# Optimization experiments

Hardware: AMD Instinct MI355X
Metric: run time of the kernel (lower is better)

Reference implementation:

```python
import jax, jax.numpy as jnp
import numpy as np

B, T, D = 8, 1024, 256
H, KD = 8, 256          # keras MHA built with key_dim=embed_dim -> per-head dim = D
FF = 1024
WIN = 64                # causal sliding window size
G = 2                   # num_global_tokens (last-k tokens of the sequence)
EPS = 1e-6
NEG = -1e9


def _mha(q_in, kv_in, Wq, bq, Wk, bk, Wv, bv, Wo, bo, mask=None):
    """Keras-style MultiHeadAttention. q_in:[B,Tq,D], kv_in:[B,Ts,D] -> [B,Tq,D]."""
    q = jnp.einsum('btd,dhk->bthk', q_in, Wq) + bq
    k = jnp.einsum('bsd,dhk->bshk', kv_in, Wk) + bk
    v = jnp.einsum('bsd,dhk->bshk', kv_in, Wv) + bv
    s = jnp.einsum('bthk,bshk->bhts', q, k) / jnp.sqrt(jnp.asarray(KD, q.dtype))
    if mask is not None:
        s = jnp.where(mask, s, jnp.asarray(NEG, s.dtype))
    a = jax.nn.softmax(s, axis=-1)
    o = jnp.einsum('bhts,bshk->bthk', a, v)
    return jnp.einsum('bthk,hkd->btd', o, Wo) + bo


def _ln(x, g, b):
    m = jnp.mean(x, axis=-1, keepdims=True)
    v = jnp.mean(jnp.square(x - m), axis=-1, keepdims=True)
    return (x - m) * jax.lax.rsqrt(v + EPS) * g + b


def setup_inputs() -> dict:
    key = jax.random.key(0)
    ks = jax.random.split(key, 32)
    sp = 1.0 / np.sqrt(D)   # proj fan-in D
    so = 1.0 / np.sqrt(H * KD)

    def mha_params(k0):
        k = jax.random.split(k0, 4)
        return dict(
            Wq=jax.random.normal(k[0], (D, H, KD), jnp.float32) * sp,
            Wk=jax.random.normal(k[1], (D, H, KD), jnp.float32) * sp,
            Wv=jax.random.normal(k[2], (D, H, KD), jnp.float32) * sp,
            Wo=jax.random.normal(k[3], (H, KD, D), jnp.float32) * so,
        )
    lp = mha_params(ks[1])
    gp = mha_params(ks[2])
    inp = {
        'x': jax.random.normal(ks[0], (B, T, D), jnp.float32),
        'lWq': lp['Wq'], 'lbq': jnp.zeros((H, KD), jnp.float32),
        'lWk': lp['Wk'], 'lbk': jnp.zeros((H, KD), jnp.float32),
        'lWv': lp['Wv'], 'lbv': jnp.zeros((H, KD), jnp.float32),
        'lWo': lp['Wo'], 'lbo': jnp.zeros((D,), jnp.float32),
        'gWq': gp['Wq'], 'gbq': jnp.zeros((H, KD), jnp.float32),
        'gWk': gp['Wk'], 'gbk': jnp.zeros((H, KD), jnp.float32),
        'gWv': gp['Wv'], 'gbv': jnp.zeros((H, KD), jnp.float32),
        'gWo': gp['Wo'], 'gbo': jnp.zeros((D,), jnp.float32),
        'fW1': jax.random.normal(ks[3], (D, FF), jnp.float32) * sp,
        'fb1': jnp.zeros((FF,), jnp.float32),
        'fW2': jax.random.normal(ks[4], (FF, D), jnp.float32) * (1.0 / np.sqrt(FF)),
        'fb2': jnp.zeros((D,), jnp.float32),
        'ln1_g': jnp.ones((D,), jnp.float32), 'ln1_b': jnp.zeros((D,), jnp.float32),
        'ln2_g': jnp.ones((D,), jnp.float32), 'ln2_b': jnp.zeros((D,), jnp.float32),
    }
    return inp


def reference(x, lWq, lbq, lWk, lbk, lWv, lbv, lWo, lbo,
              gWq, gbq, gWk, gbk, gWv, gbv, gWo, gbo,
              fW1, fb1, fW2, fb2, ln1_g, ln1_b, ln2_g, ln2_b):
    i = jnp.arange(T)[:, None]
    j = jnp.arange(T)[None, :]
    win_mask = (j <= i) & (j > i - WIN)            # [T,T]
    win_mask = win_mask[None, None]                # [1,1,T,T]

    # Local window attention (the original per-timestep loop, fused via mask).
    local = _mha(x, x, lWq, lbq, lWk, lbk, lWv, lbv, lWo, lbo, mask=win_mask)

    # Global tokens: last G tokens attend to full sequence, then tokens attend to them.
    g = x[:, T - G:, :]                            # [B,G,D]
    g2 = _mha(g, x, gWq, gbq, gWk, gbk, gWv, gbv, gWo, gbo)
    gx = _mha(x, g2, gWq, gbq, gWk, gbk, gWv, gbv, gWo, gbo)

    attn_out = local + gx
    out1 = _ln(x + attn_out, ln1_g, ln1_b)
    ffn = jnp.maximum(out1 @ fW1 + fb1, 0.0) @ fW2 + fb2
    return _ln(out1 + ffn, ln2_g, ln2_b)
```

## Files before the change

### kernel.cpp

```cpp
#include <hip/hip_runtime.h>
#include <hip/hip_bf16.h>

#define B_ 8
#define T_ 1024
#define D_ 256
#define H_ 8
#define KD_ 256
#define HK_ 2048
#define FF_ 1024
#define WIN_ 64
#define BT_ 8192
#define S6_ 6144

using bf16 = __hip_bfloat16;
typedef float f32x4 __attribute__((ext_vector_type(4)));
typedef short s16x8 __attribute__((ext_vector_type(8)));

__device__ inline float b2f(bf16 h) { return __bfloat162float(h); }
__device__ inline float bs2f(short s) {
    unsigned int u = ((unsigned int)(unsigned short)s) << 16;
    return __builtin_bit_cast(float, u);
}
__device__ inline float us2f(unsigned short s) {
    unsigned int u = ((unsigned int)s) << 16;
    return __builtin_bit_cast(float, u);
}
__device__ inline unsigned short fbits(float x) { bf16 h = __float2bfloat16(x); return __builtin_bit_cast(unsigned short, h); }

__device__ __forceinline__ void stage16(const void* g, void* l) {
    __builtin_amdgcn_global_load_lds((const __attribute__((address_space(1))) void*)g,
                                     (__attribute__((address_space(3))) void*)l, 16, 0, 0);
}

struct TJob { const float* in; bf16* out; int R; int C; int os; int tile_start; };
struct TJobs { TJob j[10]; int total; };

__global__ void transpose_all(TJobs js) {
    __shared__ float tile[32][33];
    int bid = blockIdx.x;
    int ji = 0;
    while (ji < 9 && bid >= js.j[ji + 1].tile_start) ji++;
    TJob jb = js.j[ji];
    int t = bid - jb.tile_start;
    int tiles_x = jb.C / 32;
    int cb = (t % tiles_x) * 32, rb = (t / tiles_x) * 32;
    for (int k = 0; k < 4; k++) {
        int r = threadIdx.y + k * 8;
        tile[r][threadIdx.x] = jb.in[(size_t)(rb + r) * jb.C + cb + threadIdx.x];
    }
    __syncthreads();
    for (int k = 0; k < 4; k++) {
        int r = threadIdx.y + k * 8;
        jb.out[(size_t)(cb + r) * jb.os + rb + threadIdx.x] = __float2bfloat16(tile[threadIdx.x][r]);
    }
}

__global__ __launch_bounds__(256) void concat_bias6(const float* a0, const float* a1, const float* a2,
                                                    float* out) {
    int i = blockIdx.x * 256 + threadIdx.x;
    int seg = i >> 11, off = i & 2047;
    out[i] = (seg == 0 ? a0 : seg == 1 ? a1 : a2)[off];
}

template <int MODE, int BN>
__global__ __launch_bounds__(256) void gemm128(const bf16* __restrict__ A, const bf16* __restrict__ Bt,
                                               const float* __restrict__ bias, bf16* __restrict__ C,
                                               int M, int N, int K) {
    constexpr int NF = BN / 32;
    constexpr int ABUF = 128 * 64;
    constexpr int BBUF = BN * 64;
    constexpr int BUFE = ABUF + BBUF;
    constexpr int EC = BN + 8;
    constexpr int ARENA_E = (2 * BUFE > 128 * EC) ? 2 * BUFE : 128 * EC;
    __shared__ __align__(16) bf16 arena[ARENA_E];
    const int tid = threadIdx.x;
    const int w = tid >> 6, l = tid & 63;
    const int m0 = blockIdx.y * 128, n0 = blockIdx.x * BN;
    const int wm = (w >> 1) * 64, wn = (w & 1) * (BN / 2);
    const int srow = w * 8 + (l >> 3);
    const int scol = ((l & 7) ^ (l >> 3)) * 8;
    const int ldsOff = w * 512;
    const int nt = K / 64;

    auto stageT = [&](int buf, int k0) {
        bf16* Ad = arena + buf * BUFE;
        bf16* Bd = Ad + ABUF;
#pragma unroll
        for (int j = 0; j < 4; j++)
            stage16(A + (size_t)(m0 + j * 32 + srow) * K + k0 + scol, &Ad[ldsOff + j * 2048]);
#pragma unroll
        for (int j = 0; j < NF; j++)
            stage16(Bt + (size_t)(n0 + j * 32 + srow) * K + k0 + scol, &Bd[ldsOff + j * 2048]);
    };

    f32x4 acc[4][NF] = {};
    stageT(0, 0);
    __syncthreads();
    int cur = 0;
    for (int t = 0; t < nt; t++) {
        if (t + 1 < nt) stageT(cur ^ 1, (t + 1) * 64);
        const bf16* As = arena + cur * BUFE;
        const bf16* Bs = As + ABUF;
#pragma unroll
        for (int ks = 0; ks < 2; ks++) {
            s16x8 a[4], b[NF];
#pragma unroll
            for (int mf = 0; mf < 4; mf++) {
                int ar = wm + mf * 16 + (l & 15);
                int ch = (ks * 4 + (l >> 4)) ^ (ar & 7);
                a[mf] = *(const s16x8*)&As[ar * 64 + ch * 8];
            }
#pragma unroll
            for (int nf = 0; nf < NF; nf++) {
                int br = wn + nf * 16 + (l & 15);
                int ch = (ks * 4 + (l >> 4)) ^ (br & 7);
                b[nf] = *(const s16x8*)&Bs[br * 64 + ch * 8];
            }
            __builtin_amdgcn_s_setprio(1);
#pragma unroll
            for (int mf = 0; mf < 4; mf++)
#pragma unroll
                for (int nf = 0; nf < NF; nf++)
                    acc[mf][nf] = __builtin_amdgcn_mfma_f32_16x16x32_bf16(a[mf], b[nf], acc[mf][nf], 0, 0, 0);
            __builtin_amdgcn_s_setprio(0);
        }
        __syncthreads();
        cur ^= 1;
    }
    bf16* Es = arena;
#pragma unroll
    for (int mf = 0; mf < 4; mf++)
#pragma unroll
        for (int nf = 0; nf < NF; nf++)
#pragma unroll
            for (int r = 0; r < 4; r++) {
                int row = wm + mf * 16 + (l >> 4) * 4 + r;
                int col = wn + nf * 16 + (l & 15);
                float v = acc[mf][nf][r] + bias[n0 + col];
                if (MODE == 2) v = fmaxf(v, 0.f);
                Es[row * EC + col] = __float2bfloat16(v);
            }
    __syncthreads();
    constexpr int RPC = BN / 8;
    constexpr int CPT = (128 * BN) / (256 * 8);
#pragma unroll
    for (int c = 0; c < CPT; c++) {
        int lin = c * 256 + tid;
        int row = lin / RPC, cc = lin - row * RPC;
        s16x8 v = *(const s16x8*)&Es[row * EC + cc * 8];
        *(s16x8*)(C + (size_t)(m0 + row) * N + n0 + cc * 8) = v;
    }
}

__global__ __launch_bounds__(256) void local_attn(const bf16* __restrict__ XW, bf16* __restrict__ O) {
    __shared__ bf16 U[256 * 72];
    __shared__ bf16 Ps[64][136];
    const int tid = threadIdx.x, l = tid & 63, w = tid >> 6;
    const int qt = blockIdx.x, bh = blockIdx.y;
    const int b = bh >> 3, h = bh & 7;
    const int qs = qt * 64;
    const int r0 = w * 16;
    const int lrow = tid >> 2, lc4 = (tid & 3) * 8;
    const size_t obase = (size_t)b * T_ * HK_ + h * KD_;

    s16x8 qa[8];
    {
        const bf16* qbase = XW + (size_t)(b * T_ + qs + r0 + (l & 15)) * S6_ + h * KD_ + (l >> 4) * 8;
#pragma unroll
        for (int ks = 0; ks < 8; ks++) qa[ks] = *(const s16x8*)(qbase + ks * 32);
    }

    bf16(*Ks)[264] = (bf16(*)[264])U;
    {
        int tk = qs - 64 + lrow;
        const bf16* krow = XW + (size_t)(b * T_ + tk) * S6_ + 2048 + h * KD_;
#pragma unroll
        for (int c = 0; c < 8; c++) {
            int col = lc4 + c * 32;
            uint4 val = {0, 0, 0, 0};
            if (tk >= 0) val = *(const uint4*)(krow + col);
            *(uint4*)&Ks[lrow][col] = val;
        }
    }
    __syncthreads();
    f32x4 sacc[8];
#pragma unroll
    for (int f = 0; f < 8; f++) sacc[f] = (f32x4){0.f, 0.f, 0.f, 0.f};
    __builtin_amdgcn_s_setprio(1);
#pragma unroll
    for (int nf = 0; nf < 4; nf++)
#pragma unroll
        for (int ks = 0; ks < 8; ks++) {
            s16x8 bb = *(const s16x8*)&Ks[nf * 16 + (l & 15)][ks * 32 + (l >> 4) * 8];
            sacc[nf] = __builtin_amdgcn_mfma_f32_16x16x32_bf16(qa[ks], bb, sacc[nf], 0, 0, 0);
        }
    __builtin_amdgcn_s_setprio(0);
    __syncthreads();
    {
        const bf16* krow = XW + (size_t)(b * T_ + qs + lrow) * S6_ + 2048 + h * KD_;
#pragma unroll
        for (int c = 0; c < 8; c++) {
            int col = lc4 + c * 32;
            *(uint4*)&Ks[lrow][col] = *(const uint4*)(krow + col);
        }
    }
    __syncthreads();
    __builtin_amdgcn_s_setprio(1);
#pragma unroll
    for (int nf = 0; nf < 4; nf++)
#pragma unroll
        for (int ks = 0; ks < 8; ks++) {
            s16x8 bb = *(const s16x8*)&Ks[nf * 16 + (l & 15)][ks * 32 + (l >> 4) * 8];
            sacc[4 + nf] = __builtin_amdgcn_mfma_f32_16x16x32_bf16(qa[ks], bb, sacc[4 + nf], 0, 0, 0);
        }
    __builtin_amdgcn_s_setprio(0);

    uint4 vreg[8];
    {
        int tk = qs - 64 + lrow;
        const bf16* vrow = XW + (size_t)(b * T_ + tk) * S6_ + 4096 + h * KD_;
#pragma unroll
        for (int c = 0; c < 8; c++) {
            uint4 v = {0, 0, 0, 0};
            if (tk >= 0) v = *(const uint4*)(vrow + lc4 + c * 32);
            vreg[c] = v;
        }
    }

#pragma unroll
    for (int r = 0; r < 4; r++) {
        int i = qs + r0 + (l >> 4) * 4 + r;
#pragma unroll
        for (int f = 0; f < 8; f++) {
            int j = qs - 64 + f * 16 + (l & 15);
            bool valid = (j >= 0) && (j <= i) && (j > i - WIN_);
            sacc[f][r] = valid ? sacc[f][r] * (1.f / 16.f) : -1e9f;
        }
        float mm = -1e30f;
#pragma unroll
        for (int f = 0; f < 8; f++) mm = fmaxf(mm, sacc[f][r]);
        mm = fmaxf(mm, __shfl_xor(mm, 1, 64));
        mm = fmaxf(mm, __shfl_xor(mm, 2, 64));
        mm = fmaxf(mm, __shfl_xor(mm, 4, 64));
        mm = fmaxf(mm, __shfl_xor(mm, 8, 64));
        float ss = 0.f;
#pragma unroll
        for (int f = 0; f < 8; f++) {
            float e = __expf(sacc[f][r] - mm);
            sacc[f][r] = e;
            ss += e;
        }
        ss += __shfl_xor(ss, 1, 64);
        ss += __shfl_xor(ss, 2, 64);
        ss += __shfl_xor(ss, 4, 64);
        ss += __shfl_xor(ss, 8, 64);
        float inv = 1.f / ss;
#pragma unroll
        for (int f = 0; f < 8; f++) sacc[f][r] *= inv;
    }
    __syncthreads();

    bf16(*VT)[72] = (bf16(*)[72])U;
#pragma unroll
    for (int f = 0; f < 8; f++)
#pragma unroll
        for (int r = 0; r < 4; r++)
            Ps[r0 + (l >> 4) * 4 + r][f * 16 + (l & 15)] = __float2bfloat16(sacc[f][r]);
#pragma unroll
    for (int c = 0; c < 8; c++) {
        int col = lc4 + c * 32;
        bf16 tmp[8];
        *(uint4*)tmp = vreg[c];
        for (int e = 0; e < 8; e++) VT[col + e][lrow] = tmp[e];
    }
    __syncthreads();
    {
        const bf16* vrow = XW + (size_t)(b * T_ + qs + lrow) * S6_ + 4096 + h * KD_;
#pragma unroll
        for (int c = 0; c < 8; c++) vreg[c] = *(const uint4*)(vrow + lc4 + c * 32);
    }

    f32x4 oacc[16];
#pragma unroll
    for (int nf = 0; nf < 16; nf++) oacc[nf] = (f32x4){0.f, 0.f, 0.f, 0.f};
    for (int kb = 0; kb < 2; kb++) {
#pragma unroll
        for (int ks = 0; ks < 2; ks++) {
            s16x8 a = *(const s16x8*)&Ps[r0 + (l & 15)][kb * 64 + ks * 32 + (l >> 4) * 8];
            __builtin_amdgcn_s_setprio(1);
#pragma unroll
            for (int nf = 0; nf < 16; nf++) {
                s16x8 bb = *(const s16x8*)&VT[nf * 16 + (l & 15)][ks * 32 + (l >> 4) * 8];
                oacc[nf] = __builtin_amdgcn_mfma_f32_16x16x32_bf16(a, bb, oacc[nf], 0, 0, 0);
            }
            __builtin_amdgcn_s_setprio(0);
        }
        if (kb == 0) {
            __syncthreads();
#pragma unroll
            for (int c = 0; c < 8; c++) {
                int col = lc4 + c * 32;
                bf16 tmp[8];
                *(uint4*)tmp = vreg[c];
                for (int e = 0; e < 8; e++) VT[col + e][lrow] = tmp[e];
            }
            __syncthreads();
        }
    }
#pragma unroll
    for (int nf = 0; nf < 16; nf++)
#pragma unroll
        for (int r = 0; r < 4; r++) {
            int row = r0 + (l >> 4) * 4 + r;
            int col = nf * 16 + (l & 15);
            O[obase + (size_t)(qs + row) * HK_ + col] = __float2bfloat16(oacc[nf][r]);
        }
}

__global__ __launch_bounds__(256) void qg_kernel(const float* __restrict__ x, const bf16* __restrict__ gwq_t,
                                                 const float* __restrict__ gbq, float* __restrict__ qg) {
    __shared__ float xs[256];
    int bi = blockIdx.x, ch = blockIdx.y, tid = threadIdx.x;
    int b = bi >> 1, i = bi & 1;
    xs[tid] = x[((size_t)b * T_ + (T_ - 2 + i)) * D_ + tid];
    __syncthreads();
    int hk = ch * 256 + tid;
    const bf16* wr = gwq_t + (size_t)hk * D_;
    float acc = gbq[hk];
    for (int c = 0; c < 32; c++) {
        s16x8 wv = *(const s16x8*)&wr[c * 8];
#pragma unroll
        for (int e = 0; e < 8; e++) acc += xs[c * 8 + e] * bs2f(wv[e]);
    }
    qg[(size_t)bi * HK_ + hk] = acc;
}

__global__ __launch_bounds__(256) void qk_kernel(const float* __restrict__ qg, const bf16* __restrict__ gwk_t,
                                                 const float* __restrict__ gbk, float* __restrict__ qk,
                                                 float* __restrict__ cb) {
    __shared__ float qgs[256];
    __shared__ float red[4];
    int bi = blockIdx.x, h = blockIdx.y, tid = threadIdx.x;
    qgs[tid] = qg[(size_t)bi * HK_ + h * 256 + tid];
    __syncthreads();
    float acc = 0.f;
    const bf16* wcol = gwk_t + (size_t)(h * 256) * D_ + tid;
    for (int kd = 0; kd < 256; kd++) acc += qgs[kd] * b2f(wcol[(size_t)kd * D_]);
    qk[(size_t)(bi * 8 + h) * 256 + tid] = acc;
    float pc = qgs[tid] * gbk[h * 256 + tid];
#pragma unroll
    for (int m = 32; m >= 1; m >>= 1) pc += __shfl_xor(pc, m, 64);
    if ((tid & 63) == 0) red[tid >> 6] = pc;
    __syncthreads();
    if (tid == 0) cb[bi * 8 + h] = red[0] + red[1] + red[2] + red[3];
}

__global__ __launch_bounds__(256) void conv_scores(const float* __restrict__ x, bf16* __restrict__ xb,
                                                   const float* __restrict__ qk, const float* __restrict__ cb,
                                                   float* __restrict__ sc) {
    int w = threadIdx.x >> 6, l = threadIdx.x & 63;
    int t = blockIdx.x * 4 + w;
    int b = t >> 10, tl = t & 1023;
    size_t base = (size_t)t * D_ + l * 4;
    float4 x4 = *(const float4*)(x + base);
    ushort4 o;
    o.x = fbits(x4.x); o.y = fbits(x4.y); o.z = fbits(x4.z); o.w = fbits(x4.w);
    *(ushort4*)((unsigned short*)xb + base) = o;
#pragma unroll
    for (int h = 0; h < 8; h++)
#pragma unroll
        for (int i = 0; i < 2; i++) {
            int bi = b * 2 + i;
            float4 a4 = *(const float4*)(qk + (size_t)(bi * 8 + h) * 256 + l * 4);
            float dt = x4.x * a4.x + x4.y * a4.y + x4.z * a4.z + x4.w * a4.w;
#pragma unroll
            for (int m = 32; m >= 1; m >>= 1) dt += __shfl_xor(dt, m, 64);
            if (l == 0) sc[((size_t)((b * 8 + h) * 2 + i)) * T_ + tl] = (dt + cb[bi * 8 + h]) * (1.f / 16.f);
        }
}

__global__ __launch_bounds__(256) void g2_softmax(float* __restrict__ sc) {
    __shared__ float red[4];
    int bh = blockIdx.x, tid = threadIdx.x;
    int w = tid >> 6;
    for (int i = 0; i < 2; i++) {
        float* row = &sc[((size_t)bh * 2 + i) * T_];
        float vals[4];
        float m = -1e30f;
        for (int c = 0; c < 4; c++) {
            vals[c] = row[tid + 256 * c];
            m = fmaxf(m, vals[c]);
        }
        for (int s = 32; s >= 1; s >>= 1) m = fmaxf(m, __shfl_xor(m, s, 64));
        if ((tid & 63) == 0) red[w] = m;
        __syncthreads();
        m = fmaxf(fmaxf(red[0], red[1]), fmaxf(red[2], red[3]));
        __syncthreads();
        float s = 0.f;
        for (int c = 0; c < 4; c++) {
            vals[c] = __expf(vals[c] - m);
            s += vals[c];
        }
        for (int d = 32; d >= 1; d >>= 1) s += __shfl_xor(s, d, 64);
        if ((tid & 63) == 0) red[w] = s;
        __syncthreads();
        s = red[0] + red[1] + red[2] + red[3];
        float inv = 1.f / s;
        for (int c = 0; c < 4; c++) row[tid + 256 * c] = vals[c] * inv;
        __syncthreads();
    }
}

__global__ __launch_bounds__(256) void xbar_kernel(const float* __restrict__ sc, const float* __restrict__ x,
                                                   float* __restrict__ xbar_part) {
    __shared__ float p2[2][256];
    int bh = blockIdx.x, ch = blockIdx.y;
    int b = bh >> 3;
    int tid = threadIdx.x;
    for (int i = 0; i < 2; i++) p2[i][tid] = sc[((size_t)bh * 2 + i) * T_ + ch * 256 + tid];
    __syncthreads();
    const float* xp = x + ((size_t)(b * T_ + ch * 256)) * D_ + tid;
    float a0 = 0.f, a1 = 0.f;
    for (int t = 0; t < 256; t++) {
        float xv = xp[(size_t)t * D_];
        a0 += p2[0][t] * xv;
        a1 += p2[1][t] * xv;
    }
    xbar_part[((size_t)(bh * 4 + ch) * 2 + 0) * KD_ + tid] = a0;
    xbar_part[((size_t)(bh * 4 + ch) * 2 + 1) * KD_ + tid] = a1;
}

__global__ __launch_bounds__(256) void g2_vo(const float* __restrict__ xbar_part, const bf16* __restrict__ gwv_t,
                                             const float* __restrict__ gbv, float* __restrict__ og2) {
    __shared__ float xbs[256];
    int bi = blockIdx.x, h = blockIdx.y, tid = threadIdx.x;
    int b = bi >> 1, i = bi & 1;
    int bh = b * 8 + h;
    float s = 0.f;
#pragma unroll
    for (int ch = 0; ch < 4; ch++) s += xbar_part[((size_t)(bh * 4 + ch) * 2 + i) * KD_ + tid];
    xbs[tid] = s;
    __syncthreads();
    int hk = h * 256 + tid;
    const bf16* wr = gwv_t + (size_t)hk * D_;
    float acc = gbv[hk];
    for (int c = 0; c < 32; c++) {
        s16x8 wv = *(const s16x8*)&wr[c * 8];
#pragma unroll
        for (int e = 0; e < 8; e++) acc += xbs[c * 8 + e] * bs2f(wv[e]);
    }
    og2[(size_t)bi * HK_ + hk] = acc;
}

__global__ __launch_bounds__(256) void g2_lin2(const float* __restrict__ og2, const bf16* __restrict__ gwoT,
                                               const float* __restrict__ gbo, float* __restrict__ g2buf) {
    int bi = blockIdx.x, tid = threadIdx.x;
    int d = blockIdx.y * 16 + (tid >> 4);
    int s16i = tid & 15;
    const float* ogr = og2 + (size_t)bi * 2048 + s16i * 128;
    const bf16* wr = gwoT + (size_t)d * HK_ + s16i * 128;
    float acc = 0.f;
    for (int c = 0; c < 16; c++) {
        s16x8 wv = *(const s16x8*)&wr[c * 8];
#pragma unroll
        for (int e = 0; e < 8; e++) acc += ogr[c * 8 + e] * bs2f(wv[e]);
    }
    acc += __shfl_xor(acc, 1, 64);
    acc += __shfl_xor(acc, 2, 64);
    acc += __shfl_xor(acc, 4, 64);
    acc += __shfl_xor(acc, 8, 64);
    if (s16i == 0) g2buf[(size_t)bi * 256 + d] = acc + gbo[d];
}

__global__ __launch_bounds__(256) void g2_kva2(const float* __restrict__ g2buf, const bf16* __restrict__ gwk_t,
                                               const float* __restrict__ gbk, const bf16* __restrict__ gwv_t,
                                               const float* __restrict__ gbv, const bf16* __restrict__ gwq_t,
                                               const bf16* __restrict__ gwoT, const float* __restrict__ gbq,
                                               float* __restrict__ A2, float* __restrict__ W2,
                                               float* __restrict__ c2) {
    __shared__ float g2s[256], k2s[256], v2s[256];
    __shared__ float red[4];
    int bi = blockIdx.x, h = blockIdx.y, tid = threadIdx.x;
    g2s[tid] = g2buf[(size_t)bi * 256 + tid];
    __syncthreads();
    int hk = h * 256 + tid;
    {
        const bf16* rk = &gwk_t[(size_t)hk * D_];
        const bf16* rv = &gwv_t[(size_t)hk * D_];
        float ak = gbk[hk], av = gbv[hk];
        for (int c = 0; c < 32; c++) {
            s16x8 kw = *(const s16x8*)&rk[c * 8];
            s16x8 vw = *(const s16x8*)&rv[c * 8];
#pragma unroll
            for (int e = 0; e < 8; e++) {
                float g = g2s[c * 8 + e];
                ak += g * bs2f(kw[e]);
                av += g * bs2f(vw[e]);
            }
        }
        k2s[tid] = ak;
        v2s[tid] = av;
    }
    __syncthreads();
    float accA = 0.f;
    const bf16* wq = gwq_t + (size_t)(h * 256) * D_ + tid;
    for (int kd = 0; kd < 256; kd++)
        accA += k2s[kd] * b2f(wq[(size_t)kd * D_]);
    float accW = 0.f;
    const bf16* wo = gwoT + (size_t)tid * HK_ + h * 256;
    for (int c = 0; c < 32; c++) {
        s16x8 wv = *(const s16x8*)&wo[c * 8];
#pragma unroll
        for (int e = 0; e < 8; e++) accW += v2s[c * 8 + e] * bs2f(wv[e]);
    }
    int o = (bi * 8 + h) * 256 + tid;
    A2[o] = accA;
    W2[o] = accW;
    float pc = gbq[h * 256 + tid] * k2s[tid];
#pragma unroll
    for (int m = 32; m >= 1; m >>= 1) pc += __shfl_xor(pc, m, 64);
    if ((tid & 63) == 0) red[tid >> 6] = pc;
    __syncthreads();
    if (tid == 0) c2[bi * 8 + h] = red[0] + red[1] + red[2] + red[3];
}

__global__ __launch_bounds__(256) void ln1_gx(const float* __restrict__ x, const bf16* __restrict__ attnL,
                                              const float* __restrict__ A2, const float* __restrict__ W2,
                                              const float* __restrict__ c2, const float* __restrict__ gbo,
                                              const float* __restrict__ g, const float* __restrict__ bia,
                                              bf16* __restrict__ outb) {
    int w = threadIdx.x >> 6, l = threadIdx.x & 63;
    int t = blockIdx.x * 4 + w;
    int b = t >> 10;
    size_t base = (size_t)t * D_ + l * 4;
    float4 x4 = *(const float4*)(x + base);
    float p[8][2];
#pragma unroll
    for (int h = 0; h < 8; h++)
#pragma unroll
        for (int i = 0; i < 2; i++) {
            float4 a4 = *(const float4*)(A2 + ((size_t)((b * 2 + i) * 8 + h)) * 256 + l * 4);
            float dt = x4.x * a4.x + x4.y * a4.y + x4.z * a4.z + x4.w * a4.w;
#pragma unroll
            for (int m = 32; m >= 1; m >>= 1) dt += __shfl_xor(dt, m, 64);
            p[h][i] = dt;
        }
    float4 gb = *(const float4*)(gbo + l * 4);
    float o0 = gb.x, o1 = gb.y, o2 = gb.z, o3 = gb.w;
#pragma unroll
    for (int h = 0; h < 8; h++) {
        float s0 = (p[h][0] + c2[(b * 2 + 0) * 8 + h]) * (1.f / 16.f);
        float s1 = (p[h][1] + c2[(b * 2 + 1) * 8 + h]) * (1.f / 16.f);
        float mx = fmaxf(s0, s1);
        float e0 = __expf(s0 - mx), e1 = __expf(s1 - mx);
        float inv = 1.f / (e0 + e1);
        float p0 = e0 * inv, p1 = e1 * inv;
        float4 w0 = *(const float4*)(W2 + ((size_t)((b * 2 + 0) * 8 + h)) * 256 + l * 4);
        float4 w1 = *(const float4*)(W2 + ((size_t)((b * 2 + 1) * 8 + h)) * 256 + l * 4);
        o0 += p0 * w0.x + p1 * w1.x;
        o1 += p0 * w0.y + p1 * w1.y;
        o2 += p0 * w0.z + p1 * w1.z;
        o3 += p0 * w0.w + p1 * w1.w;
    }
    ushort4 av = *(const ushort4*)((const unsigned short*)attnL + base);
    float vv[4];
    vv[0] = x4.x + us2f(av.x) + o0;
    vv[1] = x4.y + us2f(av.y) + o1;
    vv[2] = x4.z + us2f(av.z) + o2;
    vv[3] = x4.w + us2f(av.w) + o3;
    float s = vv[0] + vv[1] + vv[2] + vv[3];
#pragma unroll
    for (int m = 32; m >= 1; m >>= 1) s += __shfl_xor(s, m, 64);
    float mean = s * (1.f / 256.f);
    float q = 0.f;
#pragma unroll
    for (int e = 0; e < 4; e++) {
        float d = vv[e] - mean;
        q += d * d;
    }
#pragma unroll
    for (int m = 32; m >= 1; m >>= 1) q += __shfl_xor(q, m, 64);
    float rs = rsqrtf(q * (1.f / 256.f) + 1e-6f);
    float4 gv = *(const float4*)(g + l * 4);
    float4 biv = *(const float4*)(bia + l * 4);
    ushort4 ou;
    ou.x = fbits((vv[0] - mean) * rs * gv.x + biv.x);
    ou.y = fbits((vv[1] - mean) * rs * gv.y + biv.y);
    ou.z = fbits((vv[2] - mean) * rs * gv.z + biv.z);
    ou.w = fbits((vv[3] - mean) * rs * gv.w + biv.w);
    *(ushort4*)((unsigned short*)outb + base) = ou;
}

template <typename TA, bool HASC>
__global__ __launch_bounds__(256) void ln_kernel(const TA* __restrict__ a, const bf16* __restrict__ b2,
                                                 const bf16* __restrict__ c, const float* __restrict__ g,
                                                 const float* __restrict__ bia, float* __restrict__ outf,
                                                 bf16* __restrict__ outb) {
    int w = threadIdx.x >> 6, l = threadIdx.x & 63;
    int row = blockIdx.x * 4 + w;
    size_t base = (size_t)row * D_ + l * 4;
    float vv[4];
    if constexpr (sizeof(TA) == 4) {
        float4 av = *(const float4*)((const float*)a + base);
        vv[0] = av.x; vv[1] = av.y; vv[2] = av.z; vv[3] = av.w;
    } else {
        ushort4 av = *(const ushort4*)((const unsigned short*)a + base);
        vv[0] = us2f(av.x); vv[1] = us2f(av.y); vv[2] = us2f(av.z); vv[3] = us2f(av.w);
    }
    ushort4 bv = *(const ushort4*)((const unsigned short*)b2 + base);
    vv[0] += us2f(bv.x); vv[1] += us2f(bv.y); vv[2] += us2f(bv.z); vv[3] += us2f(bv.w);
    if constexpr (HASC) {
        ushort4 cv = *(const ushort4*)((const unsigned short*)c + base);
        vv[0] += us2f(cv.x); vv[1] += us2f(cv.y); vv[2] += us2f(cv.z); vv[3] += us2f(cv.w);
    }
    float s = vv[0] + vv[1] + vv[2] + vv[3];
#pragma unroll
    for (int m = 32; m >= 1; m >>= 1) s += __shfl_xor(s, m, 64);
    float mean = s * (1.f / 256.f);
    float q = 0.f;
#pragma unroll
    for (int e = 0; e < 4; e++) {
        float d = vv[e] - mean;
        q += d * d;
    }
#pragma unroll
    for (int m = 32; m >= 1; m >>= 1) q += __shfl_xor(q, m, 64);
    float rs = rsqrtf(q * (1.f / 256.f) + 1e-6f);
    float4 gv = *(const float4*)(g + l * 4);
    float4 biv = *(const float4*)(bia + l * 4);
    float o0 = (vv[0] - mean) * rs * gv.x + biv.x;
    float o1 = (vv[1] - mean) * rs * gv.y + biv.y;
    float o2 = (vv[2] - mean) * rs * gv.z + biv.z;
    float o3 = (vv[3] - mean) * rs * gv.w + biv.w;
    if (outf) *(float4*)(outf + base) = (float4){o0, o1, o2, o3};
    if (outb) {
        ushort4 ou;
        ou.x = fbits(o0); ou.y = fbits(o1); ou.z = fbits(o2); ou.w = fbits(o3);
        *(ushort4*)(outb + base) = ou;
    }
}

extern "C" void kernel_launch(void* const* d_in, const int* in_sizes, int n_in, void* d_out, int out_size,
                              void* d_ws, size_t ws_size, hipStream_t stream) {
    const float* x = (const float*)d_in[0];
    const float* lWq = (const float*)d_in[1];  const float* lbq = (const float*)d_in[2];
    const float* lWk = (const float*)d_in[3];  const float* lbk = (const float*)d_in[4];
    const float* lWv = (const float*)d_in[5];  const float* lbv = (const float*)d_in[6];
    const float* lWo = (const float*)d_in[7];  const float* lbo = (const float*)d_in[8];
    const float* gWq = (const float*)d_in[9];  const float* gbq = (const float*)d_in[10];
    const float* gWk = (const float*)d_in[11]; const float* gbk = (const float*)d_in[12];
    const float* gWv = (const float*)d_in[13]; const float* gbv = (const float*)d_in[14];
    const float* gWo = (const float*)d_in[15]; const float* gbo = (const float*)d_in[16];
    const float* fW1 = (const float*)d_in[17]; const float* fb1 = (const float*)d_in[18];
    const float* fW2 = (const float*)d_in[19]; const float* fb2 = (const float*)d_in[20];
    const float* ln1g = (const float*)d_in[21]; const float* ln1b = (const float*)d_in[22];
    const float* ln2g = (const float*)d_in[23]; const float* ln2b = (const float*)d_in[24];

    char* ws = (char*)d_ws;
    size_t off = 0;
    auto alloc = [&](size_t bytes) -> char* {
        char* p = ws + off;
        off = (off + bytes + 255) & ~(size_t)255;
        return p;
    };
    bf16* xb = (bf16*)alloc((size_t)BT_ * D_ * 2);
    bf16* W6 = (bf16*)alloc((size_t)S6_ * D_ * 2);
    bf16* gwq_t = (bf16*)alloc((size_t)HK_ * D_ * 2);
    bf16* gwk_t = (bf16*)alloc((size_t)HK_ * D_ * 2);
    bf16* gwv_t = (bf16*)alloc((size_t)HK_ * D_ * 2);
    bf16* woL = (bf16*)alloc((size_t)D_ * HK_ * 2);
    bf16* gwoT = (bf16*)alloc((size_t)D_ * HK_ * 2);
    bf16* fw1_t = (bf16*)alloc((size_t)FF_ * D_ * 2);
    bf16* fw2_t = (bf16*)alloc((size_t)D_ * FF_ * 2);
    float* bcat6 = (float*)alloc((size_t)S6_ * 4);
    bf16* XW = (bf16*)alloc((size_t)BT_ * S6_ * 2);
    bf16* Ob = (bf16*)alloc((size_t)BT_ * HK_ * 2);
    bf16* attnL = (bf16*)alloc((size_t)BT_ * D_ * 2);
    float* sc = (float*)alloc((size_t)B_ * H_ * 2 * T_ * 4);
    float* xbar_part = (float*)alloc((size_t)B_ * H_ * 4 * 2 * KD_ * 4);
    float* og2 = (float*)alloc((size_t)16 * HK_ * 4);
    float* g2buf = (float*)alloc((size_t)B_ * 2 * D_ * 4);
    float* qg = (float*)alloc((size_t)B_ * 2 * HK_ * 4);
    float* qk = (float*)alloc((size_t)16 * 8 * 256 * 4);
    float* cb = (float*)alloc((size_t)16 * 8 * 4);
    float* A2 = (float*)alloc((size_t)16 * 8 * 256 * 4);
    float* W2 = (float*)alloc((size_t)16 * 8 * 256 * 4);
    float* c2 = (float*)alloc((size_t)16 * 8 * 4);
    bf16* hid = XW;
    bf16* ffn = (bf16*)((char*)XW + (32u << 20));
    bf16* out1b = (bf16*)((char*)XW + (48u << 20));

    {
        TJobs js;
        int t = 0;
        auto add = [&](int i, const float* in, bf16* out, int R, int C, int os) {
            js.j[i] = {in, out, R, C, os, t};
            t += (R / 32) * (C / 32);
        };
        add(0, lWq, W6, D_, HK_, D_);
        add(1, lWk, W6 + (size_t)2048 * D_, D_, HK_, D_);
        add(2, lWv, W6 + (size_t)4096 * D_, D_, HK_, D_);
        add(3, gWq, gwq_t, D_, HK_, D_);
        add(4, gWk, gwk_t, D_, HK_, D_);
        add(5, gWv, gwv_t, D_, HK_, D_);
        add(6, lWo, woL, HK_, D_, HK_);
        add(7, gWo, gwoT, HK_, D_, HK_);
        add(8, fW1, fw1_t, D_, FF_, D_);
        add(9, fW2, fw2_t, FF_, D_, FF_);
        js.total = t;
        transpose_all<<<t, dim3(32, 8), 0, stream>>>(js);
    }
    concat_bias6<<<S6_ / 256, 256, 0, stream>>>(lbq, lbk, lbv, bcat6);
    qg_kernel<<<dim3(16, 8), 256, 0, stream>>>(x, gwq_t, gbq, qg);
    qk_kernel<<<dim3(16, 8), 256, 0, stream>>>(qg, gwk_t, gbk, qk, cb);

    conv_scores<<<BT_ / 4, 256, 0, stream>>>(x, xb, qk, cb, sc);

    gemm128<1, 128><<<dim3(S6_ / 128, BT_ / 128), 256, 0, stream>>>(xb, W6, bcat6, XW, BT_, S6_, D_);

    local_attn<<<dim3(T_ / 64, B_ * H_), 256, 0, stream>>>(XW, Ob);
    gemm128<1, 64><<<dim3(D_ / 64, BT_ / 128), 256, 0, stream>>>(Ob, woL, lbo, attnL, BT_, D_, HK_);

    g2_softmax<<<B_ * H_, 256, 0, stream>>>(sc);
    xbar_kernel<<<dim3(B_ * H_, 4), 256, 0, stream>>>(sc, x, xbar_part);
    g2_vo<<<dim3(16, 8), 256, 0, stream>>>(xbar_part, gwv_t, gbv, og2);
    g2_lin2<<<dim3(16, 16), 256, 0, stream>>>(og2, gwoT, gbo, g2buf);
    g2_kva2<<<dim3(16, 8), 256, 0, stream>>>(g2buf, gwk_t, gbk, gwv_t, gbv, gwq_t, gwoT, gbq, A2, W2, c2);

    ln1_gx<<<BT_ / 4, 256, 0, stream>>>(x, attnL, A2, W2, c2, gbo, ln1g, ln1b, out1b);
    gemm128<2, 128><<<dim3(FF_ / 128, BT_ / 128), 256, 0, stream>>>(out1b, fw1_t, fb1, hid, BT_, FF_, D_);
    gemm128<1, 64><<<dim3(D_ / 64, BT_ / 128), 256, 0, stream>>>(hid, fw2_t, fb2, ffn, BT_, D_, FF_);
    ln_kernel<bf16, false><<<BT_ / 4, 256, 0, stream>>>(out1b, ffn, nullptr, ln2g, ln2b, (float*)d_out, nullptr);
}
```

Baseline: 240.3 us.

## Fuse local attention output projection into attention kernel with per-head partials

The local attention kernel now multiplies its per-head output tile by the corresponding slice of the output projection weight inside the kernel, writing per-head bf16 partial results of size D instead of the HK-wide concatenated head output. The separate Wo GEMM is removed, and the LN1 kernel sums the eight per-head partials. The two output biases are pre-added once. This removes the 32MB Ob write/read and one GEMM launch, but adds 8x partial traffic (32MB) read in LN1, extra bf16 rounding per head, and a Wo weight read from global in every attention block.

```diff
diff --git a/kernel.cpp b/kernel.cpp
--- a/kernel.cpp
+++ b/kernel.cpp
@@ -152,7 +152,8 @@
     }
 }
 
-__global__ __launch_bounds__(256) void local_attn(const bf16* __restrict__ XW, bf16* __restrict__ O) {
+__global__ __launch_bounds__(256) void local_attn(const bf16* __restrict__ XW, const bf16* __restrict__ woL,
+                                                  bf16* __restrict__ Opart) {
     __shared__ bf16 U[256 * 72];
     __shared__ bf16 Ps[64][136];
     const int tid = threadIdx.x, l = tid & 63, w = tid >> 6;
@@ -161,7 +162,6 @@
     const int qs = qt * 64;
     const int r0 = w * 16;
     const int lrow = tid >> 2, lc4 = (tid & 3) * 8;
-    const size_t obase = (size_t)b * T_ * HK_ + h * KD_;
 
     s16x8 qa[8];
     {
@@ -307,14 +307,46 @@
             __syncthreads();
         }
     }
+
+    __syncthreads();
+    bf16(*Os)[264] = (bf16(*)[264])U;
 #pragma unroll
     for (int nf = 0; nf < 16; nf++)
 #pragma unroll
-        for (int r = 0; r < 4; r++) {
-            int row = r0 + (l >> 4) * 4 + r;
-            int col = nf * 16 + (l & 15);
-            O[obase + (size_t)(qs + row) * HK_ + col] = __float2bfloat16(oacc[nf][r]);
-        }
+        for (int r = 0; r < 4; r++)
+            Os[r0 + (l >> 4) * 4 + r][nf * 16 + (l & 15)] = __float2bfloat16(oacc[nf][r]);
+    s16x8 oa[8];
+#pragma unroll
+    for (int ks = 0; ks < 8; ks++)
+        oa[ks] = *(const s16x8*)&Os[r0 + (l & 15)][ks * 32 + (l >> 4) * 8];
+    f32x4 acc2[16];
+#pragma unroll
+    for (int nf = 0; nf < 16; nf++) acc2[nf] = (f32x4){0.f, 0.f, 0.f, 0.f};
+#pragma unroll
+    for (int nf = 0; nf < 16; nf++) {
+        const bf16* wrow = woL + (size_t)(nf * 16 + (l & 15)) * HK_ + h * KD_ + (l >> 4) * 8;
+        __builtin_amdgcn_s_setprio(1);
+#pragma unroll
+        for (int ks = 0; ks < 8; ks++) {
+            s16x8 bb = *(const s16x8*)(wrow + ks * 32);
+            acc2[nf] = __builtin_amdgcn_mfma_f32_16x16x32_bf16(oa[ks], bb, acc2[nf], 0, 0, 0);
+        }
+        __builtin_amdgcn_s_setprio(0);
+    }
+#pragma unroll
+    for (int nf = 0; nf < 16; nf++)
+#pragma unroll
+        for (int r = 0; r < 4; r++)
+            Os[r0 + (l >> 4) * 4 + r][nf * 16 + (l & 15)] = __float2bfloat16(acc2[nf][r]);
+    __syncthreads();
+    bf16* Obase = Opart + (size_t)h * BT_ * D_ + (size_t)(b * T_ + qs) * D_;
+#pragma unroll
+    for (int c = 0; c < 8; c++) {
+        int lin = c * 256 + tid;
+        int row = lin >> 5, cc = lin & 31;
+        s16x8 v = *(const s16x8*)&Os[row][cc * 8];
+        *(s16x8*)(Obase + (size_t)row * D_ + cc * 8) = v;
+    }
 }
 
 __global__ __launch_bounds__(256) void qg_kernel(const float* __restrict__ x, const bf16* __restrict__ gwq_t,
@@ -524,7 +556,7 @@
     if (tid == 0) c2[bi * 8 + h] = red[0] + red[1] + red[2] + red[3];
 }
 
-__global__ __launch_bounds__(256) void ln1_gx(const float* __restrict__ x, const bf16* __restrict__ attnL,
+__global__ __launch_bounds__(256) void ln1_gx(const float* __restrict__ x, const bf16* __restrict__ Opart,
                                               const float* __restrict__ A2, const float* __restrict__ W2,
                                               const float* __restrict__ c2, const float* __restrict__ gbo,
                                               const float* __restrict__ g, const float* __restrict__ bia,
@@ -562,12 +594,17 @@
         o2 += p0 * w0.z + p1 * w1.z;
         o3 += p0 * w0.w + p1 * w1.w;
     }
-    ushort4 av = *(const ushort4*)((const unsigned short*)attnL + base);
+    float aL0 = 0.f, aL1 = 0.f, aL2 = 0.f, aL3 = 0.f;
+#pragma unroll
+    for (int h = 0; h < 8; h++) {
+        ushort4 ov = *(const ushort4*)((const unsigned short*)Opart + (size_t)h * BT_ * D_ + base);
+        aL0 += us2f(ov.x); aL1 += us2f(ov.y); aL2 += us2f(ov.z); aL3 += us2f(ov.w);
+    }
     float vv[4];
-    vv[0] = x4.x + us2f(av.x) + o0;
-    vv[1] = x4.y + us2f(av.y) + o1;
-    vv[2] = x4.z + us2f(av.z) + o2;
-    vv[3] = x4.w + us2f(av.w) + o3;
+    vv[0] = x4.x + aL0 + o0;
+    vv[1] = x4.y + aL1 + o1;
+    vv[2] = x4.z + aL2 + o2;
+    vv[3] = x4.w + aL3 + o3;
     float s = vv[0] + vv[1] + vv[2] + vv[3];
 #pragma unroll
     for (int m = 32; m >= 1; m >>= 1) s += __shfl_xor(s, m, 64);
@@ -589,6 +626,11 @@
     ou.z = fbits((vv[2] - mean) * rs * gv.z + biv.z);
     ou.w = fbits((vv[3] - mean) * rs * gv.w + biv.w);
     *(ushort4*)((unsigned short*)outb + base) = ou;
+}
+
+__global__ __launch_bounds__(256) void add_bias2(const float* a, const float* b, float* out) {
+    int i = blockIdx.x * 256 + threadIdx.x;
+    out[i] = a[i] + b[i];
 }
 
 template <typename TA, bool HASC>
@@ -673,9 +715,9 @@
     bf16* fw1_t = (bf16*)alloc((size_t)FF_ * D_ * 2);
     bf16* fw2_t = (bf16*)alloc((size_t)D_ * FF_ * 2);
     float* bcat6 = (float*)alloc((size_t)S6_ * 4);
+    float* gbo_lbo = (float*)alloc((size_t)D_ * 4);
     bf16* XW = (bf16*)alloc((size_t)BT_ * S6_ * 2);
-    bf16* Ob = (bf16*)alloc((size_t)BT_ * HK_ * 2);
-    bf16* attnL = (bf16*)alloc((size_t)BT_ * D_ * 2);
+    bf16* Opart = (bf16*)alloc((size_t)H_ * BT_ * D_ * 2);
     float* sc = (float*)alloc((size_t)B_ * H_ * 2 * T_ * 4);
     float* xbar_part = (float*)alloc((size_t)B_ * H_ * 4 * 2 * KD_ * 4);
     float* og2 = (float*)alloc((size_t)16 * HK_ * 4);
@@ -711,6 +753,7 @@
         transpose_all<<<t, dim3(32, 8), 0, stream>>>(js);
     }
     concat_bias6<<<S6_ / 256, 256, 0, stream>>>(lbq, lbk, lbv, bcat6);
+    add_bias2<<<1, 256, 0, stream>>>(gbo, lbo, gbo_lbo);
     qg_kernel<<<dim3(16, 8), 256, 0, stream>>>(x, gwq_t, gbq, qg);
     qk_kernel<<<dim3(16, 8), 256, 0, stream>>>(qg, gwk_t, gbk, qk, cb);
 
@@ -718,8 +761,7 @@
 
     gemm128<1, 128><<<dim3(S6_ / 128, BT_ / 128), 256, 0, stream>>>(xb, W6, bcat6, XW, BT_, S6_, D_);
 
-    local_attn<<<dim3(T_ / 64, B_ * H_), 256, 0, stream>>>(XW, Ob);
-    gemm128<1, 64><<<dim3(D_ / 64, BT_ / 128), 256, 0, stream>>>(Ob, woL, lbo, attnL, BT_, D_, HK_);
+    local_attn<<<dim3(T_ / 64, B_ * H_), 256, 0, stream>>>(XW, woL, Opart);
 
     g2_softmax<<<B_ * H_, 256, 0, stream>>>(sc);
     xbar_kernel<<<dim3(B_ * H_, 4), 256, 0, stream>>>(sc, x, xbar_part);
@@ -727,7 +769,7 @@
     g2_lin2<<<dim3(16, 16), 256, 0, stream>>>(og2, gwoT, gbo, g2buf);
     g2_kva2<<<dim3(16, 8), 256, 0, stream>>>(g2buf, gwk_t, gbk, gwv_t, gbv, gwq_t, gwoT, gbq, A2, W2, c2);
 
-    ln1_gx<<<BT_ / 4, 256, 0, stream>>>(x, attnL, A2, W2, c2, gbo, ln1g, ln1b, out1b);
+    ln1_gx<<<BT_ / 4, 256, 0, stream>>>(x, Opart, A2, W2, c2, gbo_lbo, ln1g, ln1b, out1b);
     gemm128<2, 128><<<dim3(FF_ / 128, BT_ / 128), 256, 0, stream>>>(out1b, fw1_t, fb1, hid, BT_, FF_, D_);
     gemm128<1, 64><<<dim3(D_ / 64, BT_ / 128), 256, 0, stream>>>(hid, fw2_t, fb2, ffn, BT_, D_, FF_);
     ln_kernel<bf16, false><<<BT_ / 4, 256, 0, stream>>>(out1b, ffn, nullptr, ln2g, ln2b, (float*)d_out, nullptr);
```

After: 272.6 us. +13.5%, slower.
